# Optimization experiments

Measured on AMD Instinct MI355X. Metric: run time of the kernel, lower is better.

The kernel has to match this reference:

```python
import jax, jax.numpy as jnp
import numpy as np

B, S, D, H, F = 2, 2048, 768, 12, 3072
HD = D // H


def setup_inputs() -> dict:
    key = jax.random.key(0)
    ks = jax.random.split(key, 6)
    g = lambda k, sh, sc: jax.random.normal(k, sh, jnp.float32) * sc
    return {
        "x": g(ks[0], (B, S, D), 1.0),
        "mask": jnp.tril(jnp.ones((1, 1, S, S), dtype=jnp.bool_)),  # causal
        "qkv_w": g(ks[1], (3 * D, D), 0.02),
        "qkv_b": jnp.zeros((3 * D,), jnp.float32),
        "out_w": g(ks[2], (D, D), 0.02),
        "out_b": jnp.zeros((D,), jnp.float32),
        "fc1_w": g(ks[3], (F, D), 0.02),
        "fc1_b": jnp.zeros((F,), jnp.float32),
        "fc2_w": g(ks[4], (D, F), 0.02),
        "fc2_b": jnp.zeros((D,), jnp.float32),
        "ln1_w": jnp.ones((D,), jnp.float32),
        "ln1_b": jnp.zeros((D,), jnp.float32),
        "ln2_w": jnp.ones((D,), jnp.float32),
        "ln2_b": jnp.zeros((D,), jnp.float32),
    }


def _layernorm(x, w, b, eps=1e-5):
    m = x.mean(-1, keepdims=True)
    v = ((x - m) ** 2).mean(-1, keepdims=True)
    return (x - m) * jax.lax.rsqrt(v + eps) * w + b


def reference(x, mask, qkv_w, qkv_b, out_w, out_b, fc1_w, fc1_b, fc2_w, fc2_b,
              ln1_w, ln1_b, ln2_w, ln2_b):
    b, s, d = x.shape
    h = d // HD  # num_heads
    # --- pre-norm multi-head self-attention (dropout = eval/identity) ---
    hx = _layernorm(x, ln1_w, ln1_b)
    qkv = hx @ qkv_w.T + qkv_b                      # [b,s,3d]
    qkv = qkv.reshape(b, s, 3, h, HD).transpose(2, 0, 3, 1, 4)  # [3,b,h,s,hd]
    q, k, v = qkv[0], qkv[1], qkv[2]
    scale = jnp.sqrt(jnp.float32(HD))
    scores = jnp.einsum("bhqd,bhkd->bhqk", q, k) / scale  # [b,h,s,s]
    scores = jnp.where(mask, scores, -jnp.inf)
    attn = jax.nn.softmax(scores, axis=-1)
    o = jnp.einsum("bhqk,bhkd->bhqd", attn, v)      # [b,h,s,hd]
    o = o.transpose(0, 2, 1, 3).reshape(b, s, d)
    x = x + (o @ out_w.T + out_b)
    # --- pre-norm GELU feed-forward ---
    h2 = _layernorm(x, ln2_w, ln2_b)
    ff = jax.nn.gelu(h2 @ fc1_w.T + fc1_b, approximate=False) @ fc2_w.T + fc2_b
    return x + ff
```

## Files before the change

### kernel.cpp

```cpp
#include <hip/hip_runtime.h>
#include <hip/hip_bf16.h>
#include <cstdint>
#include <cstddef>

typedef __bf16 bf16;
typedef unsigned short ushort_t;
typedef __attribute__((ext_vector_type(8))) __bf16 bf16x8;
typedef __attribute__((ext_vector_type(4))) __bf16 bf16x4;
typedef __attribute__((ext_vector_type(4))) float f32x4;

#define NB 2
#define NS 2048
#define ND 768
#define NH 12
#define NF 3072
#define NT (NB * NS)

__device__ __forceinline__ f32x4 mfma16(bf16x8 a, bf16x8 b, f32x4 c) {
  return __builtin_amdgcn_mfma_f32_16x16x32_bf16(a, b, c, 0, 0, 0);
}

__device__ __forceinline__ void gl_lds16(const bf16* g, bf16* l) {
  __builtin_amdgcn_global_load_lds(
      (__attribute__((address_space(1))) void*)(uintptr_t)g,
      (__attribute__((address_space(3))) void*)l,
      16, 0, 0);
}

__device__ __forceinline__ int xcd_swz(int lin, int nwg) {
  const int q = nwg >> 3, r = nwg & 7;
  const int x = lin & 7, i = lin >> 3;
  return (x < r ? x * (q + 1) : r * (q + 1) + (x - r) * q) + i;
}

__device__ __forceinline__ float gelu_fast(float v) {
  const float u = v * (0.7978845608028654f + 0.03567740814f * v * v);
  const float e = exp2f(u * 2.885390081777927f);
  return v - v / (1.f + e);
}

__global__ __launch_bounds__(256) void sniff_kernel(
    const ushort_t* __restrict__ x, int* __restrict__ flag) {
  __shared__ int s[4];
  int bad = 0;
  for (int i = threadIdx.x; i < 4096; i += 256) {
    const int e = (x[i] >> 7) & 0xFF;
    bad |= (e >= 0xC0);
  }
  bad = __any(bad) ? 1 : 0;
  if ((threadIdx.x & 63) == 0) s[threadIdx.x >> 6] = bad;
  __syncthreads();
  if (threadIdx.x == 0) *flag = s[0] | s[1] | s[2] | s[3];
}

struct CvtArgs {
  const void* s[8];
  bf16* d[8];
  int n8[8];
  int total8;
};

__global__ __launch_bounds__(256) void cvt_all(CvtArgs a,
                                               const int* __restrict__ flag) {
  const int isf = *flag;
  const int stride = gridDim.x * 256;
  for (int i = blockIdx.x * 256 + threadIdx.x; i < a.total8; i += stride) {
    int seg = 0, off = i;
    while (off >= a.n8[seg]) { off -= a.n8[seg]; ++seg; }
    bf16x8 o;
    if (isf) {
      const float* s = (const float*)a.s[seg] + (size_t)off * 8;
      const f32x4 f0 = *(const f32x4*)s;
      const f32x4 f1 = *(const f32x4*)(s + 4);
#pragma unroll
      for (int j = 0; j < 4; ++j) {
        o[j] = (bf16)f0[j];
        o[4 + j] = (bf16)f1[j];
      }
    } else {
      o = *((const bf16x8*)a.s[seg] + off);
    }
    *((bf16x8*)a.d[seg] + off) = o;
  }
}

__global__ __launch_bounds__(256) void ln_kernel(
    const void* __restrict__ xv, const void* __restrict__ wv,
    const void* __restrict__ bv, bf16* __restrict__ y,
    const int* __restrict__ flag) {
  const int isf = *flag;
  const int row = blockIdx.x * 4 + (threadIdx.x >> 6);
  const int L = threadIdx.x & 63;
  const float* xf = (const float*)xv;
  const bf16* xh = (const bf16*)xv;
  const float* wf = (const float*)wv;
  const bf16* wh = (const bf16*)wv;
  const float* bf_ = (const float*)bv;
  const bf16* bh = (const bf16*)bv;
  const size_t base = (size_t)row * ND;
  float v[12];
  float s = 0.f, s2 = 0.f;
#pragma unroll
  for (int i = 0; i < 12; ++i) {
    const int c = L + i * 64;
    v[i] = isf ? xf[base + c] : (float)xh[base + c];
    s += v[i];
    s2 += v[i] * v[i];
  }
#pragma unroll
  for (int off = 1; off < 64; off <<= 1) {
    s += __shfl_xor(s, off);
    s2 += __shfl_xor(s2, off);
  }
  const float mean = s * (1.f / 768.f);
  const float var = s2 * (1.f / 768.f) - mean * mean;
  const float rstd = rsqrtf(var + 1e-5f);
  bf16* yr = y + base;
#pragma unroll
  for (int i = 0; i < 12; ++i) {
    const int c = L + i * 64;
    const float ww = isf ? wf[c] : (float)wh[c];
    const float bb = isf ? bf_[c] : (float)bh[c];
    yr[c] = (bf16)((v[i] - mean) * rstd * ww + bb);
  }
}

__global__ __launch_bounds__(256) void vt_kernel(
    const bf16* __restrict__ qkv, bf16* __restrict__ vT) {
  const int bh = blockIdx.y;
  const int b = bh / NH, h = bh % NH;
  const int st = blockIdx.x;
  __shared__ bf16 Vs[64 * 72];
  const int tid = threadIdx.x;
  {
    const int r = tid >> 2, c = (tid & 3) * 16;
    const bf16* src =
        qkv + (size_t)(b * NS + st * 64 + r) * (3 * ND) + 2 * ND + h * 64 + c;
    *(bf16x8*)&Vs[r * 72 + c] = *(const bf16x8*)src;
    *(bf16x8*)&Vs[r * 72 + c + 8] = *(const bf16x8*)(src + 8);
  }
  __syncthreads();
  {
    const int hd = tid >> 2, t0 = (tid & 3) * 16;
    bf16x8 o0, o1;
#pragma unroll
    for (int j = 0; j < 8; ++j) {
      o0[j] = Vs[(t0 + j) * 72 + hd];
      o1[j] = Vs[(t0 + 8 + j) * 72 + hd];
    }
    bf16* dst = vT + ((size_t)bh * 64 + hd) * NS + st * 64 + t0;
    *(bf16x8*)dst = o0;
    *(bf16x8*)(dst + 8) = o1;
  }
}

template <int EPI, int TM>
__global__ __launch_bounds__(256) void gemm_fast(
    const bf16* __restrict__ A, const bf16* __restrict__ Bt,
    const bf16* __restrict__ bias, const void* resid, void* C,
    int N, int K, int row0, const int* __restrict__ flag) {
  __shared__ bf16 As[2][TM * 32];
  __shared__ bf16 Bs[2][128 * 32];
  const int isf = (EPI == 2) ? *flag : 0;
  const int tid = threadIdx.x;
  const int w = tid >> 6, L = tid & 63;
  const int lg = L >> 4, lc = L & 15;
  const int wm = (w >> 1) * (TM / 2), wn = (w & 1) * 64;
  const int nwg = gridDim.x * gridDim.y;
  const int lin = xcd_swz(blockIdx.y * gridDim.x + blockIdx.x, nwg);
  const int bm = lin / gridDim.x, bn = lin % gridDim.x;
  const int MT = TM / 32;

  const bf16* Ab = A + (size_t)bm * TM * K;
  const bf16* Bb = Bt + (size_t)bn * 128 * K;

  const int sr = tid >> 2;
  const int sc = (tid & 3) * 8;

  f32x4 acc[MT][4];
#pragma unroll
  for (int i = 0; i < MT; ++i)
#pragma unroll
    for (int j = 0; j < 4; ++j) acc[i][j] = (f32x4){0.f, 0.f, 0.f, 0.f};

#define GF_STAGE(buf, kk)                                                   \
  do {                                                                      \
    gl_lds16(Ab + (size_t)sr * K + (kk) + sc, As[buf] + tid * 8);           \
    if (TM == 128)                                                          \
      gl_lds16(Ab + (size_t)(sr + 64) * K + (kk) + sc,                      \
               As[buf] + 2048 + tid * 8);                                   \
    gl_lds16(Bb + (size_t)sr * K + (kk) + sc, Bs[buf] + tid * 8);           \
    gl_lds16(Bb + (size_t)(sr + 64) * K + (kk) + sc,                        \
             Bs[buf] + 2048 + tid * 8);                                     \
  } while (0)

  GF_STAGE(0, 0);
  __syncthreads();
  int cur = 0;
  for (int k0 = 0; k0 < K; k0 += 32) {
    if (k0 + 32 < K) GF_STAGE(cur ^ 1, k0 + 32);

    bf16x8 af[MT], bfr[4];
#pragma unroll
    for (int mt = 0; mt < MT; ++mt)
      af[mt] = *(const bf16x8*)&As[cur][(wm + mt * 16 + lc) * 32 + lg * 8];
#pragma unroll
    for (int nt = 0; nt < 4; ++nt)
      bfr[nt] = *(const bf16x8*)&Bs[cur][(wn + nt * 16 + lc) * 32 + lg * 8];
#pragma unroll
    for (int mt = 0; mt < MT; ++mt)
#pragma unroll
      for (int nt = 0; nt < 4; ++nt)
        acc[mt][nt] = mfma16(af[mt], bfr[nt], acc[mt][nt]);

    __syncthreads();
    cur ^= 1;
  }
#undef GF_STAGE

  const float* rf = (const float*)resid;
  const bf16* rh = (const bf16*)resid;
  float* Cf = (float*)C;
  bf16* Ch = (bf16*)C;
#pragma unroll
  for (int mt = 0; mt < MT; ++mt) {
#pragma unroll
    for (int nt = 0; nt < 4; ++nt) {
      const int col = bn * 128 + wn + nt * 16 + lc;
      const float bv = (float)bias[col];
#pragma unroll
      for (int r = 0; r < 4; ++r) {
        const int row = bm * TM + wm + mt * 16 + lg * 4 + r;
        float v = acc[mt][nt][r] + bv;
        if (EPI == 1) v = gelu_fast(v);
        const size_t idx = (size_t)(row0 + row) * N + col;
        if (EPI == 2) {
          v += isf ? rf[idx] : (float)rh[idx];
          if (isf) Cf[idx] = v; else Ch[idx] = (bf16)v;
        } else {
          Ch[idx] = (bf16)v;
        }
      }
    }
  }
}

__global__ __launch_bounds__(256) void gemm_qkv(
    const bf16* __restrict__ A, const bf16* __restrict__ Bt,
    const bf16* __restrict__ bias, bf16* __restrict__ qkvout,
    bf16* __restrict__ vT) {
  const int K = ND, N = 3 * ND;
  __shared__ bf16 As[2][128 * 32];
  __shared__ bf16 Bs[2][128 * 32];
  const int tid = threadIdx.x;
  const int w = tid >> 6, L = tid & 63;
  const int lg = L >> 4, lc = L & 15;
  const int wm = (w >> 1) * 64, wn = (w & 1) * 64;
  const int nwg = gridDim.x * gridDim.y;
  const int lin = xcd_swz(blockIdx.y * gridDim.x + blockIdx.x, nwg);
  const int bm = lin / gridDim.x, bn = lin % gridDim.x;

  const bf16* Ab = A + (size_t)bm * 128 * K;
  const bf16* Bb = Bt + (size_t)bn * 128 * K;

  const int sr = tid >> 2;
  const int sc = (tid & 3) * 8;

  f32x4 acc[4][4];
#pragma unroll
  for (int i = 0; i < 4; ++i)
#pragma unroll
    for (int j = 0; j < 4; ++j) acc[i][j] = (f32x4){0.f, 0.f, 0.f, 0.f};

#define QKV_STAGE(buf, kk)                                                  \
  do {                                                                      \
    gl_lds16(Ab + (size_t)sr * K + (kk) + sc, As[buf] + tid * 8);           \
    gl_lds16(Ab + (size_t)(sr + 64) * K + (kk) + sc,                        \
             As[buf] + 2048 + tid * 8);                                     \
    gl_lds16(Bb + (size_t)sr * K + (kk) + sc, Bs[buf] + tid * 8);           \
    gl_lds16(Bb + (size_t)(sr + 64) * K + (kk) + sc,                        \
             Bs[buf] + 2048 + tid * 8);                                     \
  } while (0)

  QKV_STAGE(0, 0);
  __syncthreads();
  int cur = 0;
  for (int k0 = 0; k0 < K; k0 += 32) {
    if (k0 + 32 < K) QKV_STAGE(cur ^ 1, k0 + 32);

    bf16x8 af[4], bfr[4];
#pragma unroll
    for (int mt = 0; mt < 4; ++mt)
      af[mt] = *(const bf16x8*)&As[cur][(wm + mt * 16 + lc) * 32 + lg * 8];
#pragma unroll
    for (int nt = 0; nt < 4; ++nt)
      bfr[nt] = *(const bf16x8*)&Bs[cur][(wn + nt * 16 + lc) * 32 + lg * 8];
#pragma unroll
    for (int mt = 0; mt < 4; ++mt)
#pragma unroll
      for (int nt = 0; nt < 4; ++nt)
        acc[mt][nt] = mfma16(af[mt], bfr[nt], acc[mt][nt]);

    __syncthreads();
    cur ^= 1;
  }
#undef QKV_STAGE

#pragma unroll
  for (int mt = 0; mt < 4; ++mt) {
#pragma unroll
    for (int nt = 0; nt < 4; ++nt) {
      const int col = bn * 128 + wn + nt * 16 + lc;
      const float bv = (float)bias[col];
      if (col < 2 * ND) {
#pragma unroll
        for (int r = 0; r < 4; ++r) {
          const int row = bm * 128 + wm + mt * 16 + lg * 4 + r;
          qkvout[(size_t)row * N + col] = (bf16)(acc[mt][nt][r] + bv);
        }
      } else {
        const int colv = col - 2 * ND;
        const int h_ = colv >> 6, hd = colv & 63;
        bf16x4 pk;
#pragma unroll
        for (int r = 0; r < 4; ++r) pk[r] = (bf16)(acc[mt][nt][r] + bv);
        const int tok0 = bm * 128 + wm + mt * 16 + lg * 4;
        const int b_ = tok0 >> 11, s0 = tok0 & (NS - 1);
        *(bf16x4*)&vT[((size_t)(b_ * NH + h_) * 64 + hd) * NS + s0] = pk;
      }
    }
  }
}

template <int EPI>
__global__ __launch_bounds__(256) void gemm_bt(
    const bf16* __restrict__ A, const void* __restrict__ Bt,
    const void* __restrict__ bias, const void* resid, void* C,
    int N, int K, int row0, const int* __restrict__ flag) {
  __shared__ bf16 As[128 * 32];
  __shared__ bf16 Bs[128 * 32];
  const int isf = *flag;
  const int tid = threadIdx.x;
  const int w = tid >> 6, L = tid & 63;
  const int lg = L >> 4, lc = L & 15;
  const int wm = (w >> 1) * 64, wn = (w & 1) * 64;
  const int nwg = gridDim.x * gridDim.y;
  const int lin = xcd_swz(blockIdx.y * gridDim.x + blockIdx.x, nwg);
  const int bm = lin / gridDim.x, bn = lin % gridDim.x;

  const bf16* Ab = A + (size_t)bm * 128 * K;
  const bf16* Bth = (const bf16*)Bt + (size_t)bn * 128 * K;
  const float* Btf = (const float*)Bt + (size_t)bn * 128 * K;

  const int sr = tid >> 1;
  const int sc = (tid & 1) * 16;

  f32x4 acc[4][4];
#pragma unroll
  for (int i = 0; i < 4; ++i)
#pragma unroll
    for (int j = 0; j < 4; ++j) acc[i][j] = (f32x4){0.f, 0.f, 0.f, 0.f};

  for (int k0 = 0; k0 < K; k0 += 32) {
    const bf16* ap = Ab + (size_t)sr * K + k0 + sc;
    const bf16x8 a0 = *(const bf16x8*)ap;
    const bf16x8 a1 = *(const bf16x8*)(ap + 8);
    bf16x8 b0, b1;
    if (isf) {
      const float* bp = Btf + (size_t)sr * K + k0 + sc;
      const f32x4 f0 = *(const f32x4*)bp;
      const f32x4 f1 = *(const f32x4*)(bp + 4);
      const f32x4 f2 = *(const f32x4*)(bp + 8);
      const f32x4 f3 = *(const f32x4*)(bp + 12);
#pragma unroll
      for (int j = 0; j < 4; ++j) {
        b0[j] = (bf16)f0[j];
        b0[4 + j] = (bf16)f1[j];
        b1[j] = (bf16)f2[j];
        b1[4 + j] = (bf16)f3[j];
      }
    } else {
      const bf16* bp = Bth + (size_t)sr * K + k0 + sc;
      b0 = *(const bf16x8*)bp;
      b1 = *(const bf16x8*)(bp + 8);
    }
    __syncthreads();
    *(bf16x8*)&As[sr * 32 + sc] = a0;
    *(bf16x8*)&As[sr * 32 + sc + 8] = a1;
    *(bf16x8*)&Bs[sr * 32 + sc] = b0;
    *(bf16x8*)&Bs[sr * 32 + sc + 8] = b1;
    __syncthreads();

    bf16x8 af[4], bfr[4];
#pragma unroll
    for (int mt = 0; mt < 4; ++mt)
      af[mt] = *(const bf16x8*)&As[(wm + mt * 16 + lc) * 32 + lg * 8];
#pragma unroll
    for (int nt = 0; nt < 4; ++nt)
      bfr[nt] = *(const bf16x8*)&Bs[(wn + nt * 16 + lc) * 32 + lg * 8];
#pragma unroll
    for (int mt = 0; mt < 4; ++mt)
#pragma unroll
      for (int nt = 0; nt < 4; ++nt)
        acc[mt][nt] = mfma16(af[mt], bfr[nt], acc[mt][nt]);
  }

  const float* biasf = (const float*)bias;
  const bf16* biash = (const bf16*)bias;
  const float* rf = (const float*)resid;
  const bf16* rh = (const bf16*)resid;
  float* Cf = (float*)C;
  bf16* Ch = (bf16*)C;
#pragma unroll
  for (int mt = 0; mt < 4; ++mt) {
#pragma unroll
    for (int nt = 0; nt < 4; ++nt) {
      const int col = bn * 128 + wn + nt * 16 + lc;
      const float bv = isf ? biasf[col] : (float)biash[col];
#pragma unroll
      for (int r = 0; r < 4; ++r) {
        const int row = bm * 128 + wm + mt * 16 + lg * 4 + r;
        float v = acc[mt][nt][r] + bv;
        if (EPI == 1) v = gelu_fast(v);
        const size_t idx = (size_t)(row0 + row) * N + col;
        if (EPI == 2) {
          v += isf ? rf[idx] : (float)rh[idx];
          if (isf) Cf[idx] = v; else Ch[idx] = (bf16)v;
        } else {
          Ch[idx] = (bf16)v;
        }
      }
    }
  }
}

__global__ __launch_bounds__(256) void flash_attn_v7(
    const bf16* __restrict__ qkv, const bf16* __restrict__ vT,
    bf16* __restrict__ o) {
  const int nwg = gridDim.x * gridDim.y;
  const int lin = xcd_swz(blockIdx.y * gridDim.x + blockIdx.x, nwg);
  const int bh = lin / gridDim.x;
  const int b = bh / NH, h = bh % NH;
  const int qt = gridDim.x - 1 - (lin % gridDim.x);
  const int q0 = qt * 64;
  const int tid = threadIdx.x;
  const int w = tid >> 6, L = tid & 63;
  const int lg = L >> 4, lc = L & 15;

  __shared__ bf16 Ks[2][64 * 72];
  __shared__ bf16 Vts[2][64 * 72];
  __shared__ bf16 Ps[4][16 * 72];

  const float QSCALE = 0.18033688011112042f;
  const size_t tokq = (size_t)(b * NS + q0 + w * 16 + lc);
  const bf16* qp = qkv + tokq * (3 * ND) + h * 64 + lg * 8;
  bf16x8 qf0, qf1;
  {
    const bf16x8 qr0 = *(const bf16x8*)qp;
    const bf16x8 qr1 = *(const bf16x8*)(qp + 32);
#pragma unroll
    for (int j = 0; j < 8; ++j) {
      qf0[j] = (bf16)((float)qr0[j] * QSCALE);
      qf1[j] = (bf16)((float)qr1[j] * QSCALE);
    }
  }

  const int kr = tid >> 2, kc = (tid & 3) * 16;
  const bf16* kbase =
      qkv + (size_t)(b * NS + kr) * (3 * ND) + ND + h * 64 + kc;
  const bf16* vbase = vT + ((size_t)bh * 64 + kr) * NS + kc;

  f32x4 oacc[4];
#pragma unroll
  for (int nt = 0; nt < 4; ++nt) oacc[nt] = (f32x4){0.f, 0.f, 0.f, 0.f};
  float lacc = 0.f;

  const int nkt = qt + 1;

  bf16x8 kreg[2], vreg[2];
#pragma unroll
  for (int p = 0; p < 2; ++p) {
    kreg[p] = *(const bf16x8*)(kbase + p * 8);
    vreg[p] = *(const bf16x8*)(vbase + p * 8);
  }
  *(bf16x8*)&Ks[0][kr * 72 + kc] = kreg[0];
  *(bf16x8*)&Ks[0][kr * 72 + kc + 8] = kreg[1];
  *(bf16x8*)&Vts[0][kr * 72 + kc] = vreg[0];
  *(bf16x8*)&Vts[0][kr * 72 + kc + 8] = vreg[1];

  for (int kt = 0; kt < nkt; ++kt) {
    __syncthreads();
    const int cur = kt & 1;

    if (kt + 1 < nkt) {
      const bf16* kn = kbase + (size_t)(kt + 1) * 64 * (3 * ND);
      const bf16* vn = vbase + (size_t)(kt + 1) * 64;
#pragma unroll
      for (int p = 0; p < 2; ++p) {
        kreg[p] = *(const bf16x8*)(kn + p * 8);
        vreg[p] = *(const bf16x8*)(vn + p * 8);
      }
    }

    f32x4 s[4];
    __builtin_amdgcn_s_setprio(1);
#pragma unroll
    for (int nt = 0; nt < 4; ++nt) {
      const bf16x8 kb0 =
          *(const bf16x8*)&Ks[cur][(nt * 16 + lc) * 72 + lg * 8];
      const bf16x8 kb1 =
          *(const bf16x8*)&Ks[cur][(nt * 16 + lc) * 72 + 32 + lg * 8];
      f32x4 z = (f32x4){0.f, 0.f, 0.f, 0.f};
      s[nt] = mfma16(kb0, qf0, z);
      s[nt] = mfma16(kb1, qf1, s[nt]);
    }
    __builtin_amdgcn_s_setprio(0);
    if (kt == nkt - 1) {
#pragma unroll
      for (int nt = 0; nt < 4; ++nt)
#pragma unroll
        for (int r = 0; r < 4; ++r) {
          const int kv = nt * 16 + lg * 4 + r;
          const int qrow = w * 16 + lc;
          if (kv > qrow) s[nt][r] = -1.0e30f;
        }
    }
#pragma unroll
    for (int nt = 0; nt < 4; ++nt) {
      bf16x4 pk;
#pragma unroll
      for (int r = 0; r < 4; ++r) {
        const float p = exp2f(fminf(s[nt][r], 20.f));
        lacc += p;
        pk[r] = (bf16)p;
      }
      *(bf16x4*)&Ps[w][lc * 72 + nt * 16 + lg * 4] = pk;
    }
    const bf16x8 pa0 = *(const bf16x8*)&Ps[w][lc * 72 + lg * 8];
    const bf16x8 pa1 = *(const bf16x8*)&Ps[w][lc * 72 + 32 + lg * 8];
    __builtin_amdgcn_s_setprio(1);
#pragma unroll
    for (int nt = 0; nt < 4; ++nt) {
      const bf16x8 v0 =
          *(const bf16x8*)&Vts[cur][(nt * 16 + lc) * 72 + lg * 8];
      const bf16x8 v1 =
          *(const bf16x8*)&Vts[cur][(nt * 16 + lc) * 72 + 32 + lg * 8];
      oacc[nt] = mfma16(pa0, v0, oacc[nt]);
      oacc[nt] = mfma16(pa1, v1, oacc[nt]);
    }
    __builtin_amdgcn_s_setprio(0);

    if (kt + 1 < nkt) {
      const int nxt = cur ^ 1;
      *(bf16x8*)&Ks[nxt][kr * 72 + kc] = kreg[0];
      *(bf16x8*)&Ks[nxt][kr * 72 + kc + 8] = kreg[1];
      *(bf16x8*)&Vts[nxt][kr * 72 + kc] = vreg[0];
      *(bf16x8*)&Vts[nxt][kr * 72 + kc + 8] = vreg[1];
    }
  }

  lacc += __shfl_xor(lacc, 16);
  lacc += __shfl_xor(lacc, 32);
  float lr[4];
#pragma unroll
  for (int r = 0; r < 4; ++r) lr[r] = __shfl(lacc, lg * 4 + r);

#pragma unroll
  for (int nt = 0; nt < 4; ++nt)
#pragma unroll
    for (int r = 0; r < 4; ++r) {
      const int qrow = q0 + w * 16 + lg * 4 + r;
      const float val = oacc[nt][r] / lr[r];
      o[(size_t)(b * NS + qrow) * ND + h * 64 + nt * 16 + lc] = (bf16)val;
    }
}

__global__ __launch_bounds__(256) void flash_attn_v1(
    const bf16* __restrict__ qkv, bf16* __restrict__ o) {
  const int bh = blockIdx.y;
  const int b = bh / NH, h = bh % NH;
  const int qt = gridDim.x - 1 - blockIdx.x;
  const int q0 = qt * 64;
  const int tid = threadIdx.x;
  const int w = tid >> 6, L = tid & 63;
  const int lg = L >> 4, lc = L & 15;

  __shared__ bf16 Ks[64 * 72];
  __shared__ bf16 Vts[64 * 72];
  __shared__ bf16 Ps[4][16 * 72];

  const float QSCALE = 0.18033688011112042f;
  const size_t tokq = (size_t)(b * NS + q0 + w * 16 + lc);
  const bf16* qp = qkv + tokq * (3 * ND) + h * 64 + lg * 8;
  const bf16x8 qr0 = *(const bf16x8*)qp;
  const bf16x8 qr1 = *(const bf16x8*)(qp + 32);
  bf16x8 qf0, qf1;
#pragma unroll
  for (int j = 0; j < 8; ++j) {
    qf0[j] = (bf16)((float)qr0[j] * QSCALE);
    qf1[j] = (bf16)((float)qr1[j] * QSCALE);
  }

  f32x4 oacc[4];
#pragma unroll
  for (int nt = 0; nt < 4; ++nt) oacc[nt] = (f32x4){0.f, 0.f, 0.f, 0.f};
  float lacc[4] = {0.f, 0.f, 0.f, 0.f};

  for (int kt = 0; kt <= qt; ++kt) {
    __syncthreads();
#pragma unroll
    for (int p = 0; p < 2; ++p) {
      const int r = (p * 256 + tid) >> 3;
      const int c = (tid & 7) * 8;
      const bf16* kp =
          qkv + (size_t)(b * NS + kt * 64 + r) * (3 * ND) + ND + h * 64 + c;
      const bf16x8 k8 = *(const bf16x8*)kp;
      *(bf16x8*)&Ks[r * 72 + c] = k8;
      const bf16x8 v8 = *(const bf16x8*)(kp + ND);
#pragma unroll
      for (int j = 0; j < 8; ++j) Vts[(c + j) * 72 + r] = v8[j];
    }
    __syncthreads();

    f32x4 s[4];
#pragma unroll
    for (int nt = 0; nt < 4; ++nt) {
      const bf16x8 b0 = *(const bf16x8*)&Ks[(nt * 16 + lc) * 72 + lg * 8];
      const bf16x8 b1 = *(const bf16x8*)&Ks[(nt * 16 + lc) * 72 + 32 + lg * 8];
      f32x4 z = (f32x4){0.f, 0.f, 0.f, 0.f};
      s[nt] = mfma16(qf0, b0, z);
      s[nt] = mfma16(qf1, b1, s[nt]);
    }
    if (kt == qt) {
#pragma unroll
      for (int nt = 0; nt < 4; ++nt)
#pragma unroll
        for (int r = 0; r < 4; ++r) {
          const int qrow = w * 16 + lg * 4 + r;
          const int kcol = nt * 16 + lc;
          if (kcol > qrow) s[nt][r] = -1.0e30f;
        }
    }
#pragma unroll
    for (int nt = 0; nt < 4; ++nt)
#pragma unroll
      for (int r = 0; r < 4; ++r) {
        const float p = exp2f(fminf(s[nt][r], 20.f));
        lacc[r] += p;
        Ps[w][(lg * 4 + r) * 72 + nt * 16 + lc] = (bf16)p;
      }
    __syncthreads();

    const bf16x8 p0 = *(const bf16x8*)&Ps[w][lc * 72 + lg * 8];
    const bf16x8 p1 = *(const bf16x8*)&Ps[w][lc * 72 + 32 + lg * 8];
#pragma unroll
    for (int nt = 0; nt < 4; ++nt) {
      const bf16x8 v0 = *(const bf16x8*)&Vts[(nt * 16 + lc) * 72 + lg * 8];
      const bf16x8 v1 = *(const bf16x8*)&Vts[(nt * 16 + lc) * 72 + 32 + lg * 8];
      oacc[nt] = mfma16(p0, v0, oacc[nt]);
      oacc[nt] = mfma16(p1, v1, oacc[nt]);
    }
  }

#pragma unroll
  for (int msk = 1; msk < 16; msk <<= 1)
#pragma unroll
    for (int r = 0; r < 4; ++r) lacc[r] += __shfl_xor(lacc[r], msk);

#pragma unroll
  for (int nt = 0; nt < 4; ++nt)
#pragma unroll
    for (int r = 0; r < 4; ++r) {
      const int qrow = q0 + w * 16 + lg * 4 + r;
      const float val = oacc[nt][r] / lacc[r];
      o[(size_t)(b * NS + qrow) * ND + h * 64 + nt * 16 + lc] = (bf16)val;
    }
}

extern "C" void kernel_launch(void* const* d_in, const int* in_sizes, int n_in,
                              void* d_out, int out_size, void* d_ws,
                              size_t ws_size, hipStream_t stream) {
  const void* x = d_in[0];
  const void* qkv_w = d_in[2];
  const void* qkv_b = d_in[3];
  const void* out_w = d_in[4];
  const void* out_b = d_in[5];
  const void* fc1_w = d_in[6];
  const void* fc1_b = d_in[7];
  const void* fc2_w = d_in[8];
  const void* fc2_b = d_in[9];
  const void* ln1_w = d_in[10];
  const void* ln1_b = d_in[11];
  const void* ln2_w = d_in[12];
  const void* ln2_b = d_in[13];
  (void)in_sizes; (void)n_in; (void)out_size;

  char* ws = (char*)d_ws;
  int* flag = (int*)ws;

  sniff_kernel<<<dim3(1), 256, 0, stream>>>((const ushort_t*)x, flag);

  const size_t T1 = 58210048, T2 = 51918592, T3 = 45627136, T4 = 39335680;

  if (ws_size >= T2) {
    bf16* wq = (bf16*)(ws + 256);
    bf16* wo = wq + 1769472;
    bf16* w1 = wo + 589824;
    bf16* w2 = w1 + 2359296;
    bf16* bq = w2 + 2359296;
    bf16* bo = bq + 2304;
    bf16* b1 = bo + 768;
    bf16* b2 = b1 + 3072;
    bf16* slotA = b2 + 768;
    bf16* vT = slotA + (size_t)NT * ND;
    bf16* slotB = vT + (size_t)NT * ND;
    bf16* hx = slotA, *oat = slotA, *h2 = slotA;
    bf16* qkv = slotB;

    CvtArgs ca;
    ca.s[0] = qkv_w; ca.d[0] = wq; ca.n8[0] = 1769472 / 8;
    ca.s[1] = out_w; ca.d[1] = wo; ca.n8[1] = 589824 / 8;
    ca.s[2] = fc1_w; ca.d[2] = w1; ca.n8[2] = 2359296 / 8;
    ca.s[3] = fc2_w; ca.d[3] = w2; ca.n8[3] = 2359296 / 8;
    ca.s[4] = qkv_b; ca.d[4] = bq; ca.n8[4] = 2304 / 8;
    ca.s[5] = out_b; ca.d[5] = bo; ca.n8[5] = 768 / 8;
    ca.s[6] = fc1_b; ca.d[6] = b1; ca.n8[6] = 3072 / 8;
    ca.s[7] = fc2_b; ca.d[7] = b2; ca.n8[7] = 768 / 8;
    ca.total8 = (1769472 + 589824 + 2359296 + 2359296 + 2304 + 768 + 3072 +
                 768) / 8;
    cvt_all<<<dim3(880), 256, 0, stream>>>(ca, flag);

    ln_kernel<<<dim3(NT / 4), 256, 0, stream>>>(x, ln1_w, ln1_b, hx, flag);
    gemm_qkv<<<dim3(18, 32), 256, 0, stream>>>(hx, wq, bq, qkv, vT);
    flash_attn_v7<<<dim3(NS / 64, NB * NH), 256, 0, stream>>>(qkv, vT, oat);
    gemm_fast<2, 64><<<dim3(6, 64), 256, 0, stream>>>(
        oat, wo, bo, x, d_out, ND, ND, 0, flag);
    ln_kernel<<<dim3(NT / 4), 256, 0, stream>>>(d_out, ln2_w, ln2_b, h2, flag);
    if (ws_size >= T1) {
      bf16* ff1 = slotB;
      gemm_fast<1, 128><<<dim3(24, 32), 256, 0, stream>>>(
          h2, w1, b1, nullptr, ff1, NF, ND, 0, flag);
      gemm_fast<2, 64><<<dim3(6, 64), 256, 0, stream>>>(
          ff1, w2, b2, d_out, d_out, ND, NF, 0, flag);
    } else {
      bf16* ff1c = slotB;
      for (int c = 0; c < 2; ++c) {
        gemm_fast<1, 128><<<dim3(24, 16), 256, 0, stream>>>(
            h2 + (size_t)c * 2048 * ND, w1, b1, nullptr, ff1c, NF, ND, 0, flag);
        gemm_fast<2, 64><<<dim3(6, 32), 256, 0, stream>>>(
            ff1c, w2, b2, d_out, d_out, ND, NF, c * 2048, flag);
      }
    }
  } else if (ws_size >= T4) {
    bf16* wq = (bf16*)(ws + 256);
    bf16* wo = wq + 1769472;
    bf16* w1 = wo + 589824;
    bf16* w2 = w1 + 2359296;
    bf16* bq = w2 + 2359296;
    bf16* bo = bq + 2304;
    bf16* b1 = bo + 768;
    bf16* b2 = b1 + 3072;
    bf16* slotA = b2 + 768;
    bf16* slotB = slotA + (size_t)NT * ND;
    bf16* hx = slotA, *oat = slotA, *h2 = slotA;
    bf16* qkv = slotB;

    CvtArgs ca;
    ca.s[0] = qkv_w; ca.d[0] = wq; ca.n8[0] = 1769472 / 8;
    ca.s[1] = out_w; ca.d[1] = wo; ca.n8[1] = 589824 / 8;
    ca.s[2] = fc1_w; ca.d[2] = w1; ca.n8[2] = 2359296 / 8;
    ca.s[3] = fc2_w; ca.d[3] = w2; ca.n8[3] = 2359296 / 8;
    ca.s[4] = qkv_b; ca.d[4] = bq; ca.n8[4] = 2304 / 8;
    ca.s[5] = out_b; ca.d[5] = bo; ca.n8[5] = 768 / 8;
    ca.s[6] = fc1_b; ca.d[6] = b1; ca.n8[6] = 3072 / 8;
    ca.s[7] = fc2_b; ca.d[7] = b2; ca.n8[7] = 768 / 8;
    ca.total8 = (1769472 + 589824 + 2359296 + 2359296 + 2304 + 768 + 3072 +
                 768) / 8;
    cvt_all<<<dim3(880), 256, 0, stream>>>(ca, flag);

    ln_kernel<<<dim3(NT / 4), 256, 0, stream>>>(x, ln1_w, ln1_b, hx, flag);
    gemm_fast<0, 128><<<dim3(18, 32), 256, 0, stream>>>(
        hx, wq, bq, nullptr, qkv, 3 * ND, ND, 0, flag);
    flash_attn_v1<<<dim3(NS / 64, NB * NH), 256, 0, stream>>>(qkv, oat);
    gemm_fast<2, 64><<<dim3(6, 64), 256, 0, stream>>>(
        oat, wo, bo, x, d_out, ND, ND, 0, flag);
    ln_kernel<<<dim3(NT / 4), 256, 0, stream>>>(d_out, ln2_w, ln2_b, h2, flag);
    if (ws_size >= T3) {
      bf16* ff1 = slotB;
      gemm_fast<1, 128><<<dim3(24, 32), 256, 0, stream>>>(
          h2, w1, b1, nullptr, ff1, NF, ND, 0, flag);
      gemm_fast<2, 64><<<dim3(6, 64), 256, 0, stream>>>(
          ff1, w2, b2, d_out, d_out, ND, NF, 0, flag);
    } else {
      bf16* ff1c = slotB;
      for (int c = 0; c < 2; ++c) {
        gemm_fast<1, 128><<<dim3(24, 16), 256, 0, stream>>>(
            h2 + (size_t)c * 2048 * ND, w1, b1, nullptr, ff1c, NF, ND, 0, flag);
        gemm_fast<2, 64><<<dim3(6, 32), 256, 0, stream>>>(
            ff1c, w2, b2, d_out, d_out, ND, NF, c * 2048, flag);
      }
    }
  } else {
    const size_t szTD = (size_t)NT * ND * sizeof(bf16);
    bf16* slotA = (bf16*)(ws + 256);
    bf16* qkv = (bf16*)(ws + 256 + szTD);
    bf16* hx = slotA, *oat = slotA, *h2 = slotA;
    bf16* ff1c = qkv;

    ln_kernel<<<dim3(NT / 4), 256, 0, stream>>>(x, ln1_w, ln1_b, hx, flag);
    gemm_bt<0><<<dim3(18, 32), 256, 0, stream>>>(
        hx, qkv_w, qkv_b, nullptr, qkv, 3 * ND, ND, 0, flag);
    flash_attn_v1<<<dim3(NS / 64, NB * NH), 256, 0, stream>>>(qkv, oat);
    gemm_bt<2><<<dim3(6, 32), 256, 0, stream>>>(
        oat, out_w, out_b, x, d_out, ND, ND, 0, flag);
    ln_kernel<<<dim3(NT / 4), 256, 0, stream>>>(d_out, ln2_w, ln2_b, h2, flag);
    for (int c = 0; c < 4; ++c) {
      gemm_bt<1><<<dim3(24, 8), 256, 0, stream>>>(
          h2 + (size_t)c * 1024 * ND, fc1_w, fc1_b, nullptr, ff1c, NF, ND, 0,
          flag);
      gemm_bt<2><<<dim3(6, 8), 256, 0, stream>>>(
          ff1c, fc2_w, fc2_b, d_out, d_out, ND, NF, c * 1024, flag);
    }
  }
}
```

Baseline: 333.0 us.

## Deepen GEMM LDS pipeline to multi-buffer ring with one barrier and XOR swizzle

Replaces the double-buffered K loop in both GEMM kernels with a 3- or 5-slot LDS ring. Loads are issued one to three stages ahead, and a hand-written vmcnt wait plus a single s_barrier per iteration replaces the two __syncthreads. It also XOR-swizzles the LDS column layout on both store and fragment load to cut bank conflicts. The cost is more LDS per block, which may lower occupancy. The hard-coded vmcnt counts must match the number of loads issued per stage, or the ring reads data that has not arrived.

```diff
diff --git a/kernel.cpp b/kernel.cpp
--- a/kernel.cpp
+++ b/kernel.cpp
@@ -159,23 +159,30 @@
     const bf16* __restrict__ A, const bf16* __restrict__ Bt,
     const bf16* __restrict__ bias, const void* resid, void* C,
     int N, int K, int row0, const int* __restrict__ flag) {
-  __shared__ bf16 As[2][TM * 32];
-  __shared__ bf16 Bs[2][128 * 32];
-  const int isf = (EPI == 2) ? *flag : 0;
+  constexpr int NBUF = (TM == 64) ? 5 : 3;
+  constexpr int LOOK = NBUF - 2;
+  constexpr int MT = TM / 32;
+  __shared__ bf16 As[NBUF][TM * 32];
+  __shared__ bf16 Bs[NBUF][128 * 32];
+  int isf = 0;
+  if (EPI == 2) {
+    isf = *flag;
+    asm volatile("" ::"s"(isf));
+  }
   const int tid = threadIdx.x;
   const int w = tid >> 6, L = tid & 63;
   const int lg = L >> 4, lc = L & 15;
+  const int lgx = (lg ^ ((lc >> 1) & 3)) * 8;
   const int wm = (w >> 1) * (TM / 2), wn = (w & 1) * 64;
   const int nwg = gridDim.x * gridDim.y;
   const int lin = xcd_swz(blockIdx.y * gridDim.x + blockIdx.x, nwg);
   const int bm = lin / gridDim.x, bn = lin % gridDim.x;
-  const int MT = TM / 32;
 
   const bf16* Ab = A + (size_t)bm * TM * K;
   const bf16* Bb = Bt + (size_t)bn * 128 * K;
 
   const int sr = tid >> 2;
-  const int sc = (tid & 3) * 8;
+  const int sc = ((tid & 3) ^ ((tid >> 3) & 3)) * 8;
 
   f32x4 acc[MT][4];
 #pragma unroll
@@ -194,29 +201,43 @@
              Bs[buf] + 2048 + tid * 8);                                     \
   } while (0)
 
-  GF_STAGE(0, 0);
+#define GF_COMP(cb)                                                         \
+  do {                                                                      \
+    bf16x8 af[MT], bfr[4];                                                  \
+    _Pragma("unroll") for (int mt = 0; mt < MT; ++mt) af[mt] =              \
+        *(const bf16x8*)&As[cb][(wm + mt * 16 + lc) * 32 + lgx];            \
+    _Pragma("unroll") for (int nt = 0; nt < 4; ++nt) bfr[nt] =              \
+        *(const bf16x8*)&Bs[cb][(wn + nt * 16 + lc) * 32 + lgx];            \
+    _Pragma("unroll") for (int mt = 0; mt < MT; ++mt)                       \
+        _Pragma("unroll") for (int nt = 0; nt < 4; ++nt) acc[mt][nt] =      \
+            mfma16(af[mt], bfr[nt], acc[mt][nt]);                           \
+  } while (0)
+
+  const int nk = K >> 5;
+#pragma unroll
+  for (int s = 0; s < LOOK; ++s)
+    if (s < nk) GF_STAGE(s, s * 32);
+  int cur = 0, stg = LOOK;
+  int k = 0;
+  const int kmain = (nk > LOOK) ? nk - LOOK : 0;
+  for (; k < kmain; ++k) {
+    GF_STAGE(stg, (k + LOOK) * 32);
+    if (TM == 64)
+      asm volatile("s_waitcnt vmcnt(9)" ::: "memory");
+    else
+      asm volatile("s_waitcnt vmcnt(4)" ::: "memory");
+    asm volatile("s_barrier" ::: "memory");
+    GF_COMP(cur);
+    cur = (cur + 1 == NBUF) ? 0 : cur + 1;
+    stg = (stg + 1 == NBUF) ? 0 : stg + 1;
+  }
   __syncthreads();
-  int cur = 0;
-  for (int k0 = 0; k0 < K; k0 += 32) {
-    if (k0 + 32 < K) GF_STAGE(cur ^ 1, k0 + 32);
-
-    bf16x8 af[MT], bfr[4];
-#pragma unroll
-    for (int mt = 0; mt < MT; ++mt)
-      af[mt] = *(const bf16x8*)&As[cur][(wm + mt * 16 + lc) * 32 + lg * 8];
-#pragma unroll
-    for (int nt = 0; nt < 4; ++nt)
-      bfr[nt] = *(const bf16x8*)&Bs[cur][(wn + nt * 16 + lc) * 32 + lg * 8];
-#pragma unroll
-    for (int mt = 0; mt < MT; ++mt)
-#pragma unroll
-      for (int nt = 0; nt < 4; ++nt)
-        acc[mt][nt] = mfma16(af[mt], bfr[nt], acc[mt][nt]);
-
-    __syncthreads();
-    cur ^= 1;
+  for (; k < nk; ++k) {
+    GF_COMP(cur);
+    cur = (cur + 1 == NBUF) ? 0 : cur + 1;
   }
 #undef GF_STAGE
+#undef GF_COMP
 
   const float* rf = (const float*)resid;
   const bf16* rh = (const bf16*)resid;
@@ -250,11 +271,14 @@
     const bf16* __restrict__ bias, bf16* __restrict__ qkvout,
     bf16* __restrict__ vT) {
   const int K = ND, N = 3 * ND;
-  __shared__ bf16 As[2][128 * 32];
-  __shared__ bf16 Bs[2][128 * 32];
+  constexpr int NBUF = 3;
+  constexpr int LOOK = 1;
+  __shared__ bf16 As[NBUF][128 * 32];
+  __shared__ bf16 Bs[NBUF][128 * 32];
   const int tid = threadIdx.x;
   const int w = tid >> 6, L = tid & 63;
   const int lg = L >> 4, lc = L & 15;
+  const int lgx = (lg ^ ((lc >> 1) & 3)) * 8;
   const int wm = (w >> 1) * 64, wn = (w & 1) * 64;
   const int nwg = gridDim.x * gridDim.y;
   const int lin = xcd_swz(blockIdx.y * gridDim.x + blockIdx.x, nwg);
@@ -264,7 +288,7 @@
   const bf16* Bb = Bt + (size_t)bn * 128 * K;
 
   const int sr = tid >> 2;
-  const int sc = (tid & 3) * 8;
+  const int sc = ((tid & 3) ^ ((tid >> 3) & 3)) * 8;
 
   f32x4 acc[4][4];
 #pragma unroll
@@ -282,29 +306,38 @@
              Bs[buf] + 2048 + tid * 8);                                     \
   } while (0)
 
+#define QKV_COMP(cb)                                                        \
+  do {                                                                      \
+    bf16x8 af[4], bfr[4];                                                   \
+    _Pragma("unroll") for (int mt = 0; mt < 4; ++mt) af[mt] =               \
+        *(const bf16x8*)&As[cb][(wm + mt * 16 + lc) * 32 + lgx];            \
+    _Pragma("unroll") for (int nt = 0; nt < 4; ++nt) bfr[nt] =              \
+        *(const bf16x8*)&Bs[cb][(wn + nt * 16 + lc) * 32 + lgx];            \
+    _Pragma("unroll") for (int mt = 0; mt < 4; ++mt)                        \
+        _Pragma("unroll") for (int nt = 0; nt < 4; ++nt) acc[mt][nt] =      \
+            mfma16(af[mt], bfr[nt], acc[mt][nt]);                           \
+  } while (0)
+
+  const int nk = K >> 5;
   QKV_STAGE(0, 0);
+  int cur = 0, stg = LOOK;
+  int k = 0;
+  const int kmain = nk - LOOK;
+  for (; k < kmain; ++k) {
+    QKV_STAGE(stg, (k + LOOK) * 32);
+    asm volatile("s_waitcnt vmcnt(4)" ::: "memory");
+    asm volatile("s_barrier" ::: "memory");
+    QKV_COMP(cur);
+    cur = (cur + 1 == NBUF) ? 0 : cur + 1;
+    stg = (stg + 1 == NBUF) ? 0 : stg + 1;
+  }
   __syncthreads();
-  int cur = 0;
-  for (int k0 = 0; k0 < K; k0 += 32) {
-    if (k0 + 32 < K) QKV_STAGE(cur ^ 1, k0 + 32);
-
-    bf16x8 af[4], bfr[4];
-#pragma unroll
-    for (int mt = 0; mt < 4; ++mt)
-      af[mt] = *(const bf16x8*)&As[cur][(wm + mt * 16 + lc) * 32 + lg * 8];
-#pragma unroll
-    for (int nt = 0; nt < 4; ++nt)
-      bfr[nt] = *(const bf16x8*)&Bs[cur][(wn + nt * 16 + lc) * 32 + lg * 8];
-#pragma unroll
-    for (int mt = 0; mt < 4; ++mt)
-#pragma unroll
-      for (int nt = 0; nt < 4; ++nt)
-        acc[mt][nt] = mfma16(af[mt], bfr[nt], acc[mt][nt]);
-
-    __syncthreads();
-    cur ^= 1;
+  for (; k < nk; ++k) {
+    QKV_COMP(cur);
+    cur = (cur + 1 == NBUF) ? 0 : cur + 1;
   }
 #undef QKV_STAGE
+#undef QKV_COMP
 
 #pragma unroll
   for (int mt = 0; mt < 4; ++mt) {
```

New measurement: 329.9 us. No clear change (-0.9%).
